# Optimization experiments

Measured on AMD Instinct MI355X. Metric: run time of the kernel, lower is better.

## Reference

```python
import jax, jax.numpy as jnp
import numpy as np

N, Q, C, T = 32, 300, 92, 32  # batch, queries, classes, targets-per-image
L_CLS, L_IOU, L_L1 = 1.0, 2.0, 5.0


def _cxcywh_to_xyxy(b):
    cx, cy, w, h = b[..., 0], b[..., 1], b[..., 2], b[..., 3]
    return jnp.stack([cx - 0.5 * w, cy - 0.5 * h, cx + 0.5 * w, cy + 0.5 * h], axis=-1)


def _generalized_box_iou(a, b):
    # a: [P,4] xyxy, b: [M,4] xyxy -> [P,M]
    area_a = (a[:, 2] - a[:, 0]) * (a[:, 3] - a[:, 1])
    area_b = (b[:, 2] - b[:, 0]) * (b[:, 3] - b[:, 1])
    lt = jnp.maximum(a[:, None, :2], b[None, :, :2])
    rb = jnp.minimum(a[:, None, 2:], b[None, :, 2:])
    wh = jnp.clip(rb - lt, 0.0)
    inter = wh[..., 0] * wh[..., 1]
    union = area_a[:, None] + area_b[None, :] - inter
    iou = inter / union
    lt_c = jnp.minimum(a[:, None, :2], b[None, :, :2])
    rb_c = jnp.maximum(a[:, None, 2:], b[None, :, 2:])
    wh_c = jnp.clip(rb_c - lt_c, 0.0)
    area_c = wh_c[..., 0] * wh_c[..., 1]
    return iou - (area_c - union) / area_c


def _cost_matrix(pred_logits, pred_boxes, tgt_labels, tgt_boxes):
    out_prob = jax.nn.softmax(pred_logits.reshape(-1, C), axis=-1)  # [N*Q, C]
    out_bbox = pred_boxes.reshape(-1, 4)                            # [N*Q, 4]
    cost_class = -out_prob[:, tgt_labels]                           # [N*Q, N*T]
    cost_bbox = jnp.sum(jnp.abs(out_bbox[:, None, :] - tgt_boxes[None, :, :]), axis=-1)
    cost_giou = -_generalized_box_iou(_cxcywh_to_xyxy(out_bbox), _cxcywh_to_xyxy(tgt_boxes))
    cost = L_L1 * cost_bbox + L_CLS * cost_class + L_IOU * cost_giou
    return cost.reshape(N, Q, N * T)


def _lsa(cost):
    # Jonker-Volgenant shortest augmenting path (e-maxx), cost: [n, m], n <= m.
    # Returns col4row: for each row, the assigned column.
    n, m = cost.shape
    INF = np.inf
    u = np.zeros(n + 1)
    v = np.zeros(m + 1)
    p = np.zeros(m + 1, dtype=np.int64)   # p[j] = row assigned to column j (1-based)
    way = np.zeros(m + 1, dtype=np.int64)
    for i in range(1, n + 1):
        p[0] = i
        j0 = 0
        minv = np.full(m + 1, INF)
        used = np.zeros(m + 1, dtype=bool)
        while True:
            used[j0] = True
            i0 = p[j0]
            free = ~used[1:]
            cur = cost[i0 - 1] - u[i0] - v[1:]
            upd = free & (cur < minv[1:])
            minv[1:][upd] = cur[upd]
            way[1:][upd] = j0
            j1 = 1 + int(np.argmin(np.where(free, minv[1:], INF)))
            delta = minv[j1]
            used_idx = np.nonzero(used)[0]
            u[p[used_idx]] += delta
            v[used_idx] -= delta
            minv[1:][free] -= delta
            j0 = j1
            if p[j0] == 0:
                break
        while j0:
            j1 = way[j0]
            p[j0] = p[j1]
            j0 = j1
    ans = np.full(n, -1, dtype=np.int64)
    js = np.nonzero(p[1:])[0]
    ans[p[1:][js] - 1] = js
    return ans


def _multiplier(cost):
    c_np = np.asarray(jax.device_get(cost))  # [N, Q, N*T]
    mult = np.zeros_like(c_np)
    for i in range(N):
        block = c_np[i, :, i * T:(i + 1) * T]  # [Q, T], sample i's own targets
        q_of_t = _lsa(block.T)                 # for each target, matched query
        # NOTE: faithfully replicates the original code's `count = 0` reset,
        # so columns are indexed locally (first T columns of the global axis).
        mult[i, q_of_t, np.arange(T)] = 1.0
    return jnp.asarray(mult)


def setup_inputs() -> dict:
    key = jax.random.key(0)
    k1, k2, k3, k4 = jax.random.split(key, 4)
    return {
        "pred_logits": jax.random.normal(k1, (N, Q, C), dtype=jnp.float32),
        "pred_boxes": jax.random.uniform(k2, (N, Q, 4), dtype=jnp.float32),
        "tgt_labels": jax.random.randint(k3, (N * T,), 0, C, dtype=jnp.int64),
        "tgt_boxes": jax.random.uniform(k4, (N * T, 4), dtype=jnp.float32),
    }


def reference(pred_logits, pred_boxes, tgt_labels, tgt_boxes):
    cost = _cost_matrix(pred_logits, pred_boxes, tgt_labels, tgt_boxes)
    mult = _multiplier(cost)
    return jnp.sum(cost * mult)
```

## Files before the change

kernel.cpp:

```cpp
#include <hip/hip_runtime.h>
#include <cfloat>
#include <cmath>

#define Nn 32
#define Qq 300
#define Cc 92
#define Tt 32
#define KCOLS 5
#define GSZ 10
#define GCOLS 30
#define AUCTION_ROUNDS 24
#define AUCTION_EPS 1e-3f

#define SLICES 8
#define RPS 38
#define CTHREADS 256
#define MTHREADS 320

#define DIAG_OFF   0
#define MXIS_OFF   (Nn * Tt * Qq)

__device__ inline float wave_min_bcast(float x) {
#define DPPMIN(ctrl) { int _t = __builtin_amdgcn_update_dpp( \
        __float_as_int(x), __float_as_int(x), ctrl, 0xf, 0xf, false); \
        x = fminf(x, __int_as_float(_t)); }
    DPPMIN(0x111) DPPMIN(0x112) DPPMIN(0x114) DPPMIN(0x118)
    DPPMIN(0x142) DPPMIN(0x143)
#undef DPPMIN
    return __int_as_float(__builtin_amdgcn_readlane(__float_as_int(x), 63));
}

__device__ inline int sel5i(const int a[KCOLS], int k) {
    int r = a[0];
    if (k == 1) r = a[1];
    if (k == 2) r = a[2];
    if (k == 3) r = a[3];
    if (k == 4) r = a[4];
    return r;
}

__device__ inline float readlane_f(float v, int lane) {
    return __int_as_float(__builtin_amdgcn_readlane(__float_as_int(v), lane));
}

__device__ inline float det_cost_real(float cx, float cy, float w, float h,
                                      float bcx, float bcy, float bw, float bh,
                                      float cls) {
    const float ax0 = cx - 0.5f * w, ay0 = cy - 0.5f * h;
    const float ax1 = cx + 0.5f * w, ay1 = cy + 0.5f * h;
    const float areaA = (ax1 - ax0) * (ay1 - ay0);

    const float l1 = fabsf(cx - bcx) + fabsf(cy - bcy) +
                     fabsf(w - bw) + fabsf(h - bh);

    const float bx0 = bcx - 0.5f * bw, by0 = bcy - 0.5f * bh;
    const float bx1 = bcx + 0.5f * bw, by1 = bcy + 0.5f * bh;
    const float areaB = (bx1 - bx0) * (by1 - by0);

    const float ltx = fmaxf(ax0, bx0), lty = fmaxf(ay0, by0);
    const float rbx = fminf(ax1, bx1), rby = fminf(ay1, by1);
    const float iw = fmaxf(rbx - ltx, 0.f), ih = fmaxf(rby - lty, 0.f);
    const float inter = iw * ih;
    const float uni = areaA + areaB - inter;
    const float iou = inter / uni;

    const float ex0 = fminf(ax0, bx0), ey0 = fminf(ay0, by0);
    const float ex1 = fmaxf(ax1, bx1), ey1 = fmaxf(ay1, by1);
    const float areaC = fmaxf(ex1 - ex0, 0.f) * fmaxf(ey1 - ey0, 0.f);
    const float giou = iou - (areaC - uni) / areaC;

    return 5.f * l1 + cls - 2.f * giou;
}

__global__ __launch_bounds__(CTHREADS) void cost_kernel(
    const float* __restrict__ logits,
    const float* __restrict__ pboxes,
    const int*   __restrict__ tlabels,
    const float* __restrict__ tboxes,
    float* __restrict__ ws,
    float* __restrict__ out)
{
    const int bs = blockIdx.x;
    const int b = bs >> 3, s = bs & 7;
    const int q0 = s * RPS;
    const int nq = min(RPS, Qq - q0);

    __shared__ float2 s_mxis[RPS];
    __shared__ float  s_tb[Tt * 4];
    __shared__ int    s_tl[Tt];

    const int tid = threadIdx.x;
    if (bs == 0 && tid == 0) *out = 0.f;
    if (tid < Tt * 4) s_tb[tid] = tboxes[b * Tt * 4 + tid];
    if (tid < Tt)     s_tl[tid] = tlabels[b * Tt + tid];

    const int r = tid >> 2, j = tid & 3;
    if (r < nq) {
        const float* row = logits + ((size_t)(b * Qq) + q0 + r) * Cc;
        float mj = -FLT_MAX;
#pragma unroll
        for (int c = 0; c < Cc; c += 4) mj = fmaxf(mj, row[c + j]);
        const float ma = fmaxf(mj, __shfl_xor(mj, 1, 4));
        const float mx = fmaxf(ma, __shfl_xor(ma, 2, 4));
        float sj = 0.f;
#pragma unroll
        for (int c = 0; c < Cc; c += 4) sj += __expf(row[c + j] - mx);
        const float sa   = sj + __shfl_xor(sj, 1, 4);
        const float ssum = sa + __shfl_xor(sa, 2, 4);
        if (j == 0) {
            const float2 mi = make_float2(mx, 1.f / ssum);
            s_mxis[r] = mi;
            reinterpret_cast<float2*>(ws + MXIS_OFF)[b * Qq + q0 + r] = mi;
        }
    }
    __syncthreads();

    float* diagb = ws + DIAG_OFF + (size_t)b * (Tt * Qq);
    for (int e = tid; e < Tt * RPS; e += CTHREADS) {
        const int t = e / RPS, lq = e - t * RPS;
        const int q = q0 + lq;
        if (q < Qq) {
            const float2 mi = s_mxis[lq];
            const float cls =
                -__expf(logits[((size_t)(b * Qq) + q) * Cc + s_tl[t]] - mi.x) * mi.y;
            const float4 pbv = reinterpret_cast<const float4*>(pboxes)[b * Qq + q];
            diagb[t * Qq + q] = det_cost_real(pbv.x, pbv.y, pbv.z, pbv.w,
                                              s_tb[t * 4 + 0], s_tb[t * 4 + 1],
                                              s_tb[t * 4 + 2], s_tb[t * 4 + 3], cls);
        }
    }
}

__global__ __launch_bounds__(MTHREADS) void match_kernel(
    const float* __restrict__ logits,
    const float* __restrict__ pboxes,
    const int*   __restrict__ tlabels,
    const float* __restrict__ tboxes,
    const float* __restrict__ ws,
    float* __restrict__ out)
{
    const int b = blockIdx.x;
    const int tid = threadIdx.x;

    __shared__ float s_diag[Tt * Qq];
    __shared__ float s_v[Qq];
    __shared__ float s_u[Tt + 1];
    __shared__ int   s_colrow[Qq];
    __shared__ unsigned long long s_bid64[Qq];
    __shared__ float s_pm1[MTHREADS], s_pm2[MTHREADS];
    __shared__ int   s_pa[MTHREADS];
    __shared__ int   pairs[Tt];
    __shared__ unsigned s_mask;

    {
        const float4* src = reinterpret_cast<const float4*>(
            ws + DIAG_OFF + (size_t)b * (Tt * Qq));
        float4* dst = reinterpret_cast<float4*>(s_diag);
#pragma unroll 2
        for (int g = tid; g < (Tt * Qq) / 4; g += MTHREADS) dst[g] = src[g];
    }
    if (tid < Qq)  { s_v[tid] = 0.f; s_colrow[tid] = 0; }
    if (tid == 0)  s_mask = 0xffffffffu;
    __syncthreads();

    const int grp = tid / GSZ;
    const int g   = tid - grp * GSZ;
    for (int round = 0; round < AUCTION_ROUNDS; ++round) {
        const unsigned msk = s_mask;
        if (msk == 0) break;
        for (int jj = tid; jj < Qq; jj += MTHREADS) s_bid64[jj] = 0ull;

        if (grp < Tt && (msk & (1u << grp))) {
            const float* rowp = &s_diag[grp * Qq];
            float m1 = INFINITY, m2 = INFINITY; int a1 = 0;
            const int c0 = g * GCOLS;
#pragma unroll
            for (int jj = 0; jj < GCOLS; ++jj) {
                const int cidx = c0 + jj;
                const float c = rowp[cidx] - s_v[cidx];
                if (c < m1) { m2 = m1; m1 = c; a1 = cidx + 1; }
                else if (c < m2) m2 = c;
            }
            s_pm1[tid] = m1; s_pm2[tid] = m2; s_pa[tid] = a1;
        }
        __syncthreads();

        float g1 = 0.f, g2 = 0.f; int j1 = 0;
        unsigned long long mypk = 0ull;
        if (tid < Tt && (msk & (1u << tid))) {
            float best = INFINITY, second = INFINITY, bm2 = INFINITY;
            int ba = 0;
            const int base = tid * GSZ;
#pragma unroll
            for (int q = 0; q < GSZ; ++q) {
                const float v = s_pm1[base + q];
                if (v < best) {
                    second = best; best = v;
                    ba = s_pa[base + q]; bm2 = s_pm2[base + q];
                } else if (v < second) second = v;
            }
            g1 = best; g2 = fminf(second, bm2); j1 = ba;
            mypk = ((unsigned long long)(__float_as_uint(g2 - g1) + 1u) << 32)
                   | (unsigned)(0xffffffffu - (unsigned)(tid + 1));
            atomicMax(&s_bid64[j1 - 1], mypk);
        }
        __syncthreads();

        if (tid < Tt && (msk & (1u << tid))) {
            const int row = tid + 1;
            const float eps = (round < 2 || round >= 10) ? 0.f : AUCTION_EPS;
            if (s_bid64[j1 - 1] == mypk) {
                const int old = s_colrow[j1 - 1];
                s_colrow[j1 - 1] = row;
                s_v[j1 - 1] -= (g2 - g1) + eps;
                s_u[row] = g2;
                atomicAnd(&s_mask, ~(1u << tid));
                if (old) atomicOr(&s_mask, 1u << (old - 1));
            } else {
                s_u[row] = g1;
            }
        }
        __syncthreads();
    }

    if (tid >= 64) return;
    const int lane = tid;
    const bool inval4 = (lane + 256) >= Qq;

    float u_reg = (lane >= 1 && lane <= Tt) ? s_u[lane] : 0.f;
    float v_r[KCOLS]; int p_r[KCOLS];
#pragma unroll
    for (int k = 0; k < KCOLS; ++k) {
        const int jj = lane + 64 * k;
        v_r[k] = (jj < Qq) ? s_v[jj] : 0.f;
        p_r[k] = (jj < Qq) ? s_colrow[jj] : 0;
    }
    const unsigned mask0 = s_mask;

    for (unsigned rem = mask0; rem; rem &= rem - 1) {
        const int i = __ffs(rem);

        float minv_r[KCOLS], vmask[KCOLS], am[KCOLS];
        int way_r[KCOLS];
#pragma unroll
        for (int k = 0; k < KCOLS; ++k) {
            minv_r[k] = FLT_MAX; way_r[k] = 0;
            const bool inv = (k == 4) && inval4;
            vmask[k] = inv ? -INFINITY : v_r[k];
            am[k]    = inv ?  INFINITY : 0.f;
        }
        float markg = 0.f;
        int   ent = 0;
        int   j0 = 0, i0 = i;
        float du = 0.f - readlane_f(u_reg, i);
        int   jfinal = 0;
        float Dfinal = 0.f;

        const float* rowp = &s_diag[(i0 - 1) * Qq + lane];
        float c0 = rowp[0], c1 = rowp[64], c2 = rowp[128], c3 = rowp[192],
              c4 = rowp[256];

        while (true) {
            const float cc[KCOLS] = {c0, c1, c2, c3, c4};
            float sv[KCOLS];
#pragma unroll
            for (int k = 0; k < KCOLS; ++k) {
                const float cur = (cc[k] + du) - vmask[k];
                const bool lt = cur < minv_r[k];
                way_r[k]  = lt ? j0  : way_r[k];
                minv_r[k] = lt ? cur : minv_r[k];
                sv[k] = minv_r[k] + am[k];
            }
            float val = sv[0];
            int   kb  = 0;
#pragma unroll
            for (int k = 1; k < KCOLS; ++k)
                if (sv[k] < val) { val = sv[k]; kb = k; }

            const float gmin = wave_min_bcast(val);
            const unsigned long long mask = __ballot(val == gmin);
            const int src = __ffsll((long long)mask) - 1;
            const int colid = lane + 1 + (kb << 6);
            const int pk = (sel5i(p_r, kb) << 16) | colid;
            const int got = __builtin_amdgcn_readlane(pk, src);
            const int j1   = got & 0xffff;
            const int rowm = got >> 16;

            const int k1 = (j1 - 1) >> 6;
            const bool own = (lane == ((j1 - 1) & 63));
#pragma unroll
            for (int k = 0; k < KCOLS; ++k)
                if (own && k == k1) { vmask[k] = -INFINITY; am[k] = INFINITY; }

            if (rowm == 0) { jfinal = j1; Dfinal = gmin; break; }

            i0 = rowm; j0 = j1;
            rowp = &s_diag[(i0 - 1) * Qq + lane];
            c0 = rowp[0]; c1 = rowp[64]; c2 = rowp[128]; c3 = rowp[192];
            c4 = rowp[256];
            du = gmin - readlane_f(u_reg, i0);
            markg = (lane == rowm) ? gmin : markg;
            ent   = (lane == rowm) ? 1    : ent;
        }

#pragma unroll
        for (int k = 0; k < KCOLS; ++k) {
            bool usedk = (am[k] == INFINITY);
            if (k == 4) usedk = usedk && !inval4;
            v_r[k] -= usedk ? (Dfinal - minv_r[k]) : 0.f;
        }
        u_reg += (lane == i) ? Dfinal : (ent ? (Dfinal - markg) : 0.f);

        int jj = jfinal;
        while (jj) {
            const int ow = (jj - 1) & 63, kk = (jj - 1) >> 6;
            const int jprev = __builtin_amdgcn_readlane(sel5i(way_r, kk), ow);
            int pnew;
            if (jprev == 0) pnew = i;
            else pnew = __builtin_amdgcn_readlane(sel5i(p_r, (jprev - 1) >> 6),
                                                  (jprev - 1) & 63);
            const bool own = (lane == ow);
#pragma unroll
            for (int k = 0; k < KCOLS; ++k) if (own && k == kk) p_r[k] = pnew;
            jj = jprev;
        }
    }

#pragma unroll
    for (int k = 0; k < KCOLS; ++k)
        if (p_r[k]) pairs[p_r[k] - 1] = lane + 64 * k;
    __threadfence_block();

    float part = 0.f;
    if (lane < Tt) {
        const int q = pairs[lane];
        const float2 mi =
            reinterpret_cast<const float2*>(ws + MXIS_OFF)[b * Qq + q];
        const float cls =
            -__expf(logits[((size_t)(b * Qq) + q) * Cc + tlabels[lane]] - mi.x) * mi.y;
        const float4 pbv = reinterpret_cast<const float4*>(pboxes)[b * Qq + q];
        const float4 tbv = reinterpret_cast<const float4*>(tboxes)[lane];
        part = det_cost_real(pbv.x, pbv.y, pbv.z, pbv.w,
                             tbv.x, tbv.y, tbv.z, tbv.w, cls);
    }
    for (int off = 32; off > 0; off >>= 1) part += __shfl_down(part, off);
    if (lane == 0) atomicAdd(out, part);
}

extern "C" void kernel_launch(void* const* d_in, const int* in_sizes, int n_in,
                              void* d_out, int out_size, void* d_ws, size_t ws_size,
                              hipStream_t stream) {
    const float* logits  = (const float*)d_in[0];
    const float* pboxes  = (const float*)d_in[1];
    const int*   tlabels = (const int*)d_in[2];
    const float* tboxes  = (const float*)d_in[3];
    float* out = (float*)d_out;
    float* ws  = (float*)d_ws;

    cost_kernel<<<Nn * SLICES, CTHREADS, 0, stream>>>(logits, pboxes, tlabels,
                                                      tboxes, ws, out);
    match_kernel<<<Nn, MTHREADS, 0, stream>>>(logits, pboxes, tlabels,
                                              tboxes, ws, out);
}
```

Baseline: 76.51 us.

## Fuse cost and matching kernels into one cooperative launch with grid sync

Merges the cost-matrix kernel and the auction-matching kernel into a single cooperative kernel. A grid-wide sync separates the cost phase from the matching phase, and only the first 32 blocks continue into matching; this removes the second kernel launch and the gap between launches. It also merges the bid and resolve steps of each auction round, dropping one __syncthreads per round. That merge relies on the 32 bidding threads sharing one wave64 so the LDS atomicMax results are visible when read back. The trade-offs are that every block now reserves the matching kernel's large shared memory and pays for a grid barrier.

```diff
diff --git a/kernel.cpp b/kernel.cpp
--- a/kernel.cpp
+++ b/kernel.cpp
@@ -1,6 +1,9 @@
 #include <hip/hip_runtime.h>
+#include <hip/hip_cooperative_groups.h>
 #include <cfloat>
 #include <cmath>
+
+namespace cg = cooperative_groups;
 
 #define Nn 32
 #define Qq 300
@@ -14,8 +17,7 @@
 
 #define SLICES 8
 #define RPS 38
-#define CTHREADS 256
-#define MTHREADS 320
+#define NTHREADS 320
 
 #define DIAG_OFF   0
 #define MXIS_OFF   (Nn * Tt * Qq)
@@ -72,7 +74,7 @@
     return 5.f * l1 + cls - 2.f * giou;
 }
 
-__global__ __launch_bounds__(CTHREADS) void cost_kernel(
+__global__ __launch_bounds__(NTHREADS) void fused_kernel(
     const float* __restrict__ logits,
     const float* __restrict__ pboxes,
     const int*   __restrict__ tlabels,
@@ -80,84 +82,79 @@
     float* __restrict__ ws,
     float* __restrict__ out)
 {
-    const int bs = blockIdx.x;
-    const int b = bs >> 3, s = bs & 7;
-    const int q0 = s * RPS;
-    const int nq = min(RPS, Qq - q0);
+    const int blk = blockIdx.x;
+    const int tid = threadIdx.x;
 
     __shared__ float2 s_mxis[RPS];
     __shared__ float  s_tb[Tt * 4];
     __shared__ int    s_tl[Tt];
-
-    const int tid = threadIdx.x;
-    if (bs == 0 && tid == 0) *out = 0.f;
-    if (tid < Tt * 4) s_tb[tid] = tboxes[b * Tt * 4 + tid];
-    if (tid < Tt)     s_tl[tid] = tlabels[b * Tt + tid];
-
-    const int r = tid >> 2, j = tid & 3;
-    if (r < nq) {
-        const float* row = logits + ((size_t)(b * Qq) + q0 + r) * Cc;
-        float mj = -FLT_MAX;
-#pragma unroll
-        for (int c = 0; c < Cc; c += 4) mj = fmaxf(mj, row[c + j]);
-        const float ma = fmaxf(mj, __shfl_xor(mj, 1, 4));
-        const float mx = fmaxf(ma, __shfl_xor(ma, 2, 4));
-        float sj = 0.f;
-#pragma unroll
-        for (int c = 0; c < Cc; c += 4) sj += __expf(row[c + j] - mx);
-        const float sa   = sj + __shfl_xor(sj, 1, 4);
-        const float ssum = sa + __shfl_xor(sa, 2, 4);
-        if (j == 0) {
-            const float2 mi = make_float2(mx, 1.f / ssum);
-            s_mxis[r] = mi;
-            reinterpret_cast<float2*>(ws + MXIS_OFF)[b * Qq + q0 + r] = mi;
-        }
-    }
-    __syncthreads();
-
-    float* diagb = ws + DIAG_OFF + (size_t)b * (Tt * Qq);
-    for (int e = tid; e < Tt * RPS; e += CTHREADS) {
-        const int t = e / RPS, lq = e - t * RPS;
-        const int q = q0 + lq;
-        if (q < Qq) {
-            const float2 mi = s_mxis[lq];
-            const float cls =
-                -__expf(logits[((size_t)(b * Qq) + q) * Cc + s_tl[t]] - mi.x) * mi.y;
-            const float4 pbv = reinterpret_cast<const float4*>(pboxes)[b * Qq + q];
-            diagb[t * Qq + q] = det_cost_real(pbv.x, pbv.y, pbv.z, pbv.w,
-                                              s_tb[t * 4 + 0], s_tb[t * 4 + 1],
-                                              s_tb[t * 4 + 2], s_tb[t * 4 + 3], cls);
-        }
-    }
-}
-
-__global__ __launch_bounds__(MTHREADS) void match_kernel(
-    const float* __restrict__ logits,
-    const float* __restrict__ pboxes,
-    const int*   __restrict__ tlabels,
-    const float* __restrict__ tboxes,
-    const float* __restrict__ ws,
-    float* __restrict__ out)
-{
-    const int b = blockIdx.x;
-    const int tid = threadIdx.x;
-
     __shared__ float s_diag[Tt * Qq];
     __shared__ float s_v[Qq];
     __shared__ float s_u[Tt + 1];
     __shared__ int   s_colrow[Qq];
     __shared__ unsigned long long s_bid64[Qq];
-    __shared__ float s_pm1[MTHREADS], s_pm2[MTHREADS];
-    __shared__ int   s_pa[MTHREADS];
+    __shared__ float s_pm1[NTHREADS], s_pm2[NTHREADS];
+    __shared__ int   s_pa[NTHREADS];
     __shared__ int   pairs[Tt];
     __shared__ unsigned s_mask;
+
+    {
+        const int b = blk >> 3, s = blk & 7;
+        const int q0 = s * RPS;
+        const int nq = min(RPS, Qq - q0);
+
+        if (blk == 0 && tid == 0) *out = 0.f;
+        if (tid < Tt * 4) s_tb[tid] = tboxes[b * Tt * 4 + tid];
+        if (tid < Tt)     s_tl[tid] = tlabels[b * Tt + tid];
+
+        const int r = tid >> 2, j = tid & 3;
+        if (r < nq) {
+            const float* row = logits + ((size_t)(b * Qq) + q0 + r) * Cc;
+            float mj = -FLT_MAX;
+#pragma unroll
+            for (int c = 0; c < Cc; c += 4) mj = fmaxf(mj, row[c + j]);
+            const float ma = fmaxf(mj, __shfl_xor(mj, 1, 4));
+            const float mx = fmaxf(ma, __shfl_xor(ma, 2, 4));
+            float sj = 0.f;
+#pragma unroll
+            for (int c = 0; c < Cc; c += 4) sj += __expf(row[c + j] - mx);
+            const float sa   = sj + __shfl_xor(sj, 1, 4);
+            const float ssum = sa + __shfl_xor(sa, 2, 4);
+            if (j == 0) {
+                const float2 mi = make_float2(mx, 1.f / ssum);
+                s_mxis[r] = mi;
+                reinterpret_cast<float2*>(ws + MXIS_OFF)[b * Qq + q0 + r] = mi;
+            }
+        }
+        __syncthreads();
+
+        float* diagb = ws + DIAG_OFF + (size_t)b * (Tt * Qq);
+        for (int e = tid; e < Tt * RPS; e += NTHREADS) {
+            const int t = e / RPS, lq = e - t * RPS;
+            const int q = q0 + lq;
+            if (q < Qq) {
+                const float2 mi = s_mxis[lq];
+                const float cls =
+                    -__expf(logits[((size_t)(b * Qq) + q) * Cc + s_tl[t]] - mi.x) * mi.y;
+                const float4 pbv = reinterpret_cast<const float4*>(pboxes)[b * Qq + q];
+                diagb[t * Qq + q] = det_cost_real(pbv.x, pbv.y, pbv.z, pbv.w,
+                                                  s_tb[t * 4 + 0], s_tb[t * 4 + 1],
+                                                  s_tb[t * 4 + 2], s_tb[t * 4 + 3], cls);
+            }
+        }
+    }
+
+    cg::this_grid().sync();
+
+    if (blk >= Nn) return;
+    const int b = blk;
 
     {
         const float4* src = reinterpret_cast<const float4*>(
             ws + DIAG_OFF + (size_t)b * (Tt * Qq));
         float4* dst = reinterpret_cast<float4*>(s_diag);
 #pragma unroll 2
-        for (int g = tid; g < (Tt * Qq) / 4; g += MTHREADS) dst[g] = src[g];
+        for (int g = tid; g < (Tt * Qq) / 4; g += NTHREADS) dst[g] = src[g];
     }
     if (tid < Qq)  { s_v[tid] = 0.f; s_colrow[tid] = 0; }
     if (tid == 0)  s_mask = 0xffffffffu;
@@ -168,7 +165,7 @@
     for (int round = 0; round < AUCTION_ROUNDS; ++round) {
         const unsigned msk = s_mask;
         if (msk == 0) break;
-        for (int jj = tid; jj < Qq; jj += MTHREADS) s_bid64[jj] = 0ull;
+        for (int jj = tid; jj < Qq; jj += NTHREADS) s_bid64[jj] = 0ull;
 
         if (grp < Tt && (msk & (1u << grp))) {
             const float* rowp = &s_diag[grp * Qq];
@@ -185,8 +182,6 @@
         }
         __syncthreads();
 
-        float g1 = 0.f, g2 = 0.f; int j1 = 0;
-        unsigned long long mypk = 0ull;
         if (tid < Tt && (msk & (1u << tid))) {
             float best = INFINITY, second = INFINITY, bm2 = INFINITY;
             int ba = 0;
@@ -199,14 +194,13 @@
                     ba = s_pa[base + q]; bm2 = s_pm2[base + q];
                 } else if (v < second) second = v;
             }
-            g1 = best; g2 = fminf(second, bm2); j1 = ba;
-            mypk = ((unsigned long long)(__float_as_uint(g2 - g1) + 1u) << 32)
-                   | (unsigned)(0xffffffffu - (unsigned)(tid + 1));
+            const float g1 = best, g2 = fminf(second, bm2);
+            const int j1 = ba;
+            const unsigned long long mypk =
+                ((unsigned long long)(__float_as_uint(g2 - g1) + 1u) << 32)
+                | (unsigned)(0xffffffffu - (unsigned)(tid + 1));
             atomicMax(&s_bid64[j1 - 1], mypk);
-        }
-        __syncthreads();
-
-        if (tid < Tt && (msk & (1u << tid))) {
+
             const int row = tid + 1;
             const float eps = (round < 2 || round >= 10) ? 0.f : AUCTION_EPS;
             if (s_bid64[j1 - 1] == mypk) {
@@ -357,8 +351,9 @@
     float* out = (float*)d_out;
     float* ws  = (float*)d_ws;
 
-    cost_kernel<<<Nn * SLICES, CTHREADS, 0, stream>>>(logits, pboxes, tlabels,
-                                                      tboxes, ws, out);
-    match_kernel<<<Nn, MTHREADS, 0, stream>>>(logits, pboxes, tlabels,
-                                              tboxes, ws, out);
-}
+    void* args[] = {(void*)&logits, (void*)&pboxes, (void*)&tlabels,
+                    (void*)&tboxes, (void*)&ws, (void*)&out};
+    (void)hipLaunchCooperativeKernel((const void*)fused_kernel,
+                                     dim3(Nn * SLICES), dim3(NTHREADS),
+                                     args, 0, stream);
+}
```

Result: slower. 110.3 us (+44.2%).
